# Kernel tuning notes

Hardware: AMD Instinct MI355X
Metric: run time of the kernel (lower is better)

## Reference

```python
import jax, jax.numpy as jnp
import numpy as np

B, D, H, K = 8192, 768, 16384, 32


def _topk_activation(z, k):
    # keep values >= k-th largest per row, zero the rest (dim=1 top-k)
    top_vals = jax.lax.top_k(z, k)[0]          # [B, k]
    thresh = top_vals[:, -1:]                  # [B, 1]
    return jnp.where(z >= thresh, z, jnp.zeros_like(z))


def setup_inputs() -> dict:
    key = jax.random.key(0)
    k1, k2, k3, k4 = jax.random.split(key, 4)
    x = jax.random.normal(k1, (B, D), dtype=jnp.float32)
    # encoder/decoder weights row-normalized as in _init_weights (orthogonal init then F.normalize dim=1)
    W_enc = jax.random.normal(k2, (H, D), dtype=jnp.float32)
    W_enc = W_enc / jnp.linalg.norm(W_enc, axis=1, keepdims=True)
    W_dec = jax.random.normal(k3, (D, H), dtype=jnp.float32)
    W_dec = W_dec / jnp.linalg.norm(W_dec, axis=1, keepdims=True)
    b_pre = 0.01 * jax.random.normal(k4, (D,), dtype=jnp.float32)  # geometric median stand-in
    return {"x": x, "W_enc": W_enc, "W_dec": W_dec, "b_pre": b_pre, "k_sparse": K}


def reference(x, W_enc, W_dec, b_pre, k_sparse):
    # x: [B, D]; single SAE (num_saes=1)
    xc = x - b_pre                                   # subtract pre-bias
    z = jnp.einsum('bd,hd->bh', xc, W_enc)           # encoder (no bias): [B, H]
    encoded = _topk_activation(z, k_sparse)          # top-k sparse hidden
    decoded = jnp.einsum('bh,dh->bd', encoded, W_dec) + b_pre  # decoder + b_pre
    # original returns (hidden_states, reconstructions) lists; num_saes=1
    return (encoded, decoded)
```

## Files before the change

### kernel.cpp

```cpp
#include <hip/hip_runtime.h>
#include <hip/hip_bf16.h>
#include <stdint.h>

#define B_ROWS 8192
#define D_DIM  768
#define H_DIM  16384

typedef _Float16 f16x8 __attribute__((ext_vector_type(8)));
typedef float    f32x4 __attribute__((ext_vector_type(4)));

typedef const __attribute__((address_space(1))) void gas_void;
typedef __attribute__((address_space(3))) void las_void;

union F16U { _Float16 h; unsigned short u; };
union V16U { f16x8 v; uint4 u4; };


#define CAPR   512
#define CUTSIG 2.0f
#define DELTA  1.2e-2f
#define WCAP   48
#define OUTC   64

__global__ __launch_bounds__(256)
void rownorm_kernel(const float* __restrict__ x, const float* __restrict__ bp,
                    float* __restrict__ cut, int* __restrict__ cnt)
{
    const int row = blockIdx.x;
    const int tid = threadIdx.x;
    float v = 0.0f;
    for (int d = tid; d < D_DIM; d += 256) {
        float t = x[(size_t)row * D_DIM + d] - bp[d];
        v += t * t;
    }
#pragma unroll
    for (int off = 32; off >= 1; off >>= 1)
        v += __shfl_down(v, off);
    __shared__ float sw[4];
    if ((tid & 63) == 0) sw[tid >> 6] = v;
    __syncthreads();
    if (tid == 0) {
        cut[row] = CUTSIG * sqrtf((sw[0] + sw[1] + sw[2] + sw[3]) * (1.0f / D_DIM));
        cnt[row] = 0;
    }
}

__global__ __launch_bounds__(256)
void conv_x_kernel(const float* __restrict__ x, const float* __restrict__ bp,
                   _Float16* __restrict__ xo)
{
    size_t e = ((size_t)blockIdx.x * 256 + threadIdx.x) * 8;
    int k = (int)(e % D_DIM);
    float4 a0 = *(const float4*)&x[e];
    float4 a1 = *(const float4*)&x[e + 4];
    float4 b0 = *(const float4*)&bp[k];
    float4 b1 = *(const float4*)&bp[k + 4];
    V16U r;
    r.v[0] = (_Float16)(a0.x - b0.x); r.v[1] = (_Float16)(a0.y - b0.y);
    r.v[2] = (_Float16)(a0.z - b0.z); r.v[3] = (_Float16)(a0.w - b0.w);
    r.v[4] = (_Float16)(a1.x - b1.x); r.v[5] = (_Float16)(a1.y - b1.y);
    r.v[6] = (_Float16)(a1.z - b1.z); r.v[7] = (_Float16)(a1.w - b1.w);
    *(uint4*)&xo[e] = r.u4;
}

__global__ __launch_bounds__(256)
void conv_w_kernel(const float* __restrict__ w, _Float16* __restrict__ wo)
{
    size_t e = ((size_t)blockIdx.x * 256 + threadIdx.x) * 8;
    float4 a0 = *(const float4*)&w[e];
    float4 a1 = *(const float4*)&w[e + 4];
    V16U r;
    r.v[0] = (_Float16)a0.x; r.v[1] = (_Float16)a0.y;
    r.v[2] = (_Float16)a0.z; r.v[3] = (_Float16)a0.w;
    r.v[4] = (_Float16)a1.x; r.v[5] = (_Float16)a1.y;
    r.v[6] = (_Float16)a1.z; r.v[7] = (_Float16)a1.w;
    *(uint4*)&wo[e] = r.u4;
}

__global__ __launch_bounds__(512, 2)
void mfma_gemm_extract(const _Float16* __restrict__ A,
                       const _Float16* __restrict__ Bw,
                       const float* __restrict__ cut,
                       float* __restrict__ z,
                       int* __restrict__ cnt,
                       uint32_t* __restrict__ cand)
{
    __shared__ char smem[65536];

    const int bid = blockIdx.x;
    const int swz = (bid & 7) * 256 + (bid >> 3);
    const int mt  = swz & 31;
    const int nt  = swz >> 5;

    const int tid  = threadIdx.x;
    const int w    = tid >> 6;
    const int lane = tid & 63;
    const int wr   = w >> 2;
    const int wc   = w & 3;

    f32x4 acc[8][4];
#pragma unroll
    for (int i = 0; i < 8; ++i)
#pragma unroll
        for (int j = 0; j < 4; ++j) acc[i][j] = (f32x4)(0.0f);

    const int s_rowin = lane >> 2;
    const size_t s_koff = (size_t)(((lane & 3) ^ ((lane >> 3) & 3))) * 8;

    auto stage = [&](int buf, int k0) {
#pragma unroll
        for (int i = 0; i < 2; ++i) {
            const int grp = w * 2 + i;
            const _Float16* ga = A  + (size_t)(mt * 256 + grp * 16 + s_rowin) * D_DIM + k0 + s_koff;
            const _Float16* gb = Bw + (size_t)(nt * 256 + grp * 16 + s_rowin) * D_DIM + k0 + s_koff;
            __builtin_amdgcn_global_load_lds((gas_void*)ga,
                (las_void*)(smem + buf * 32768 + grp * 1024), 16, 0, 0);
            __builtin_amdgcn_global_load_lds((gas_void*)gb,
                (las_void*)(smem + buf * 32768 + 16384 + grp * 1024), 16, 0, 0);
        }
    };

    const int rslot = (((lane >> 4) ^ ((lane >> 1) & 3)) << 4);
    const int rlow  = lane & 15;

    stage(0, 0);
    __syncthreads();

    int cur = 0;
    for (int t = 0; t < 24; ++t) {
        if (t + 1 < 24) stage(cur ^ 1, (t + 1) * 32);

        const char* bA = smem + cur * 32768;
        const char* bB = bA + 16384;
        f16x8 a[8], b[4];
#pragma unroll
        for (int fi = 0; fi < 8; ++fi)
            a[fi] = *(const f16x8*)(bA + ((wr * 128 + fi * 16 + rlow) << 6) + rslot);
#pragma unroll
        for (int fj = 0; fj < 4; ++fj)
            b[fj] = *(const f16x8*)(bB + ((wc * 64 + fj * 16 + rlow) << 6) + rslot);
#pragma unroll
        for (int fi = 0; fi < 8; ++fi)
#pragma unroll
            for (int fj = 0; fj < 4; ++fj)
                acc[fi][fj] = __builtin_amdgcn_mfma_f32_16x16x32_f16(a[fi], b[fj], acc[fi][fj], 0, 0, 0);

        __syncthreads();
        cur ^= 1;
    }

#pragma unroll
    for (int fi = 0; fi < 8; ++fi) {
        const int grow0 = mt * 256 + wr * 128 + fi * 16 + (lane >> 4) * 4;
        float cut4[4];
#pragma unroll
        for (int q = 0; q < 4; ++q) cut4[q] = cut[grow0 + q];
#pragma unroll
        for (int fj = 0; fj < 4; ++fj) {
            const int gcol = nt * 256 + wc * 64 + fj * 16 + (lane & 15);
#pragma unroll
            for (int q = 0; q < 4; ++q) {
                float val = acc[fi][fj][q];
                if (val >= cut4[q]) {
                    const int grow = grow0 + q;
                    int pos = atomicAdd(&cnt[grow], 1);
                    if (pos < CAPR) {
                        F16U fu; fu.h = (_Float16)val;
                        cand[(size_t)grow * CAPR + pos] =
                            ((uint32_t)fu.u << 16) | (uint32_t)gcol;
                    }
                }
            }
        }
    }

    const float4 z4 = make_float4(0.f, 0.f, 0.f, 0.f);
#pragma unroll
    for (int it = 0; it < 32; ++it) {
        *(float4*)&z[(size_t)(mt * 256 + w + it * 8) * H_DIM + nt * 256 + lane * 4] = z4;
    }
}

__global__ __launch_bounds__(256)
void select_kernel(const float* __restrict__ x,
                   const float* __restrict__ We,
                   const float* __restrict__ bp,
                   const int* __restrict__ cnt,
                   const uint32_t* __restrict__ cand,
                   float* __restrict__ z,
                   int* __restrict__ sel_idx,
                   float* __restrict__ sel_val,
                   int* __restrict__ sel_cnt,
                   const int* __restrict__ kptr)
{
    const int row = blockIdx.x;
    const int tid = threadIdx.x;
    const int K   = min(max(*kptr, 1), OUTC);

    __shared__ float          v[CAPR];
    __shared__ unsigned short hh[CAPR];
    __shared__ unsigned char  csel[CAPR];
    __shared__ float  xs[D_DIM];
    __shared__ int    worig[WCAP];
    __shared__ double wzd[WCAP];
    __shared__ float  sv32;
    __shared__ int    sA, swcnt, snsel;

    if (tid == 0) { sA = 0; swcnt = 0; snsel = 0; }
    const int n = min(cnt[row], CAPR);

    for (int d = tid; d < D_DIM; d += 256) xs[d] = x[(size_t)row * D_DIM + d];

    for (int c = tid; c < n; c += 256) {
        uint32_t p = cand[(size_t)row * CAPR + c];
        F16U fu; fu.u = (unsigned short)(p >> 16);
        v[c]  = (float)fu.h;
        hh[c] = (unsigned short)(p & 0xFFFF);
    }
    __syncthreads();

    if (n <= K) {
        for (int c = tid; c < n; c += 256) csel[c] = 1;
        __syncthreads();
    } else {
        for (int c = tid; c < n; c += 256) {
            float vc = v[c];
            int g = 0, e = 0;
            for (int j = 0; j < n; ++j) {
                float u = v[j];
                g += (u > vc);
                e += (u == vc);
            }
            if (g <= K - 1 && K - 1 < g + e) sv32 = vc;
        }
        __syncthreads();
        const float hi = sv32 + DELTA, lo = sv32 - DELTA;

        for (int c = tid; c < n; c += 256) {
            float vc = v[c];
            unsigned char s = 0;
            if (vc > hi) { s = 1; atomicAdd(&sA, 1); }
            else if (vc >= lo) {
                int m = atomicAdd(&swcnt, 1);
                if (m < WCAP) worig[m] = c;
            }
            csel[c] = s;
        }
        __syncthreads();

        const int wcnt = min(swcnt, WCAP);
        const int wave = tid >> 6;
        const int lane = tid & 63;
        for (int m = wave; m < wcnt; m += 4) {
            const int h = hh[worig[m]];
            const float* wr = We + (size_t)h * D_DIM;
            double s = 0.0;
#pragma unroll
            for (int q = 0; q < 12; ++q) {
                int d = lane * 12 + q;
                s += ((double)xs[d] - (double)bp[d]) * (double)wr[d];
            }
#pragma unroll
            for (int off = 32; off >= 1; off >>= 1)
                s += __shfl_down(s, off);
            if (lane == 0) wzd[m] = s;
        }
        __syncthreads();

        if (tid == 0) {
            int need = K - sA;
            if (need < 0) need = 0;
            if (need > wcnt) need = wcnt;
            for (int m = 0; m < wcnt; ++m) {
                int g = 0;
                for (int j = 0; j < wcnt; ++j) g += (wzd[j] > wzd[m]);
                if (g < need) {
                    csel[worig[m]] = 1;
                    v[worig[m]] = (float)wzd[m];
                }
            }
        }
        __syncthreads();
    }

    for (int c = tid; c < n; c += 256) {
        if (csel[c]) {
            int p = atomicAdd(&snsel, 1);
            if (p < OUTC) {
                const int h = hh[c];
                sel_idx[(size_t)row * OUTC + p] = h;
                sel_val[(size_t)row * OUTC + p] = v[c];
                z[(size_t)row * H_DIM + h] = v[c];
            }
        }
    }
    __syncthreads();
    if (tid == 0) sel_cnt[row] = min(snsel, OUTC);
}

__global__ __launch_bounds__(256)
void transpose_f16_kernel(const float* __restrict__ Wd, _Float16* __restrict__ Wt)
{
    __shared__ float t[32][33];
    const int hb = blockIdx.x * 32;
    const int db = blockIdx.y * 32;
    const int tx = threadIdx.x & 31;
    const int ty = threadIdx.x >> 5;
#pragma unroll
    for (int q = 0; q < 4; ++q)
        t[ty + q * 8][tx] = Wd[(size_t)(db + ty + q * 8) * H_DIM + hb + tx];
    __syncthreads();
#pragma unroll
    for (int q = 0; q < 4; ++q)
        Wt[(size_t)(hb + ty + q * 8) * D_DIM + db + tx] = (_Float16)t[tx][ty + q * 8];
}

__global__ __launch_bounds__(256)
void dec16_kernel(const _Float16* __restrict__ Wt,
                  const int* __restrict__ sel_cnt,
                  const int* __restrict__ sel_idx,
                  const float* __restrict__ sel_val,
                  const float* __restrict__ bp,
                  float* __restrict__ out_dec)
{
    const int row = blockIdx.x;
    const int tid = threadIdx.x;
    __shared__ int   sidx[OUTC];
    __shared__ float sval[OUTC];
    const int c = sel_cnt[row];
    if (tid < c) { sidx[tid] = sel_idx[(size_t)row * OUTC + tid];
                   sval[tid] = sel_val[(size_t)row * OUTC + tid]; }
    __syncthreads();

    float a0 = bp[tid], a1 = bp[tid + 256], a2 = bp[tid + 512];
    for (int k = 0; k < c; ++k) {
        const float vv = sval[k];
        const _Float16* wr = Wt + (size_t)sidx[k] * D_DIM;
        a0 += vv * (float)wr[tid];
        a1 += vv * (float)wr[tid + 256];
        a2 += vv * (float)wr[tid + 512];
    }
    float* o = out_dec + (size_t)row * D_DIM;
    o[tid] = a0; o[tid + 256] = a1; o[tid + 512] = a2;
}


#define BM 128
#define BN 128
#define BK 32

__global__ __launch_bounds__(256)
void enc_gemm_kernel(const float* __restrict__ x,
                     const float* __restrict__ We,
                     const float* __restrict__ bp,
                     float* __restrict__ z)
{
    __shared__ float As[BK][BM + 4];
    __shared__ float Bs[BK][BN + 4];

    const int mt  = blockIdx.x % (B_ROWS / BM);
    const int nt  = blockIdx.x / (B_ROWS / BM);
    const int tid = threadIdx.x;
    const int tx  = tid & 15;
    const int ty  = tid >> 4;
    const int lr = tid >> 3;
    const int lc = (tid & 7) * 4;

    float acc[8][8];
#pragma unroll
    for (int i = 0; i < 8; ++i)
#pragma unroll
        for (int j = 0; j < 8; ++j) acc[i][j] = 0.0f;

    for (int k0 = 0; k0 < D_DIM; k0 += BK) {
        const float4 bp4 = *(const float4*)&bp[k0 + lc];
#pragma unroll
        for (int s = 0; s < 4; ++s) {
            const int r = lr + s * 32;
            float4 a4 = *(const float4*)&x[(size_t)(mt * BM + r) * D_DIM + k0 + lc];
            As[lc + 0][r] = a4.x - bp4.x;
            As[lc + 1][r] = a4.y - bp4.y;
            As[lc + 2][r] = a4.z - bp4.z;
            As[lc + 3][r] = a4.w - bp4.w;
            float4 b4 = *(const float4*)&We[(size_t)(nt * BN + r) * D_DIM + k0 + lc];
            Bs[lc + 0][r] = b4.x;
            Bs[lc + 1][r] = b4.y;
            Bs[lc + 2][r] = b4.z;
            Bs[lc + 3][r] = b4.w;
        }
        __syncthreads();

#pragma unroll 8
        for (int kk = 0; kk < BK; ++kk) {
            float a[8], b[8];
            *(float4*)&a[0] = *(const float4*)&As[kk][ty * 4];
            *(float4*)&a[4] = *(const float4*)&As[kk][64 + ty * 4];
            *(float4*)&b[0] = *(const float4*)&Bs[kk][tx * 4];
            *(float4*)&b[4] = *(const float4*)&Bs[kk][64 + tx * 4];
#pragma unroll
            for (int i = 0; i < 8; ++i)
#pragma unroll
                for (int j = 0; j < 8; ++j)
                    acc[i][j] += a[i] * b[j];
        }
        __syncthreads();
    }

#pragma unroll
    for (int i = 0; i < 8; ++i) {
        const int rloc = (i < 4) ? (ty * 4 + i) : (64 + ty * 4 + (i - 4));
        const size_t row = (size_t)(mt * BM + rloc);
        float4 v0 = make_float4(acc[i][0], acc[i][1], acc[i][2], acc[i][3]);
        float4 v1 = make_float4(acc[i][4], acc[i][5], acc[i][6], acc[i][7]);
        *(float4*)&z[row * H_DIM + nt * BN + tx * 4]      = v0;
        *(float4*)&z[row * H_DIM + nt * BN + 64 + tx * 4] = v1;
    }
}

#define CAP  1024
#define WCAP3 64

__global__ __launch_bounds__(256)
void topk_kernel(float* __restrict__ z,
                 const float* __restrict__ x,
                 const float* __restrict__ We,
                 const float* __restrict__ bp,
                 int* __restrict__ ws_cnt,
                 int* __restrict__ ws_idx,
                 float* __restrict__ ws_val,
                 const int* __restrict__ kptr)
{
    const int row = blockIdx.x;
    const int tid = threadIdx.x;
    const int K   = min(max(*kptr, 1), OUTC);
    float* zr = z + (size_t)row * H_DIM;

    __shared__ float cval[CAP];
    __shared__ int   cidx[CAP];
    __shared__ unsigned char csel3[CAP];
    __shared__ int   worig3[WCAP3];
    __shared__ double wzd3[WCAP3];
    __shared__ int   oidx[OUTC];
    __shared__ float oval[OUTC];
    __shared__ int   scount, swcnt3, sA3, souts;
    __shared__ float sv32f;

    if (tid == 0) { scount = 0; swcnt3 = 0; sA3 = 0; souts = 0; }
    __syncthreads();

    for (int j4 = tid; j4 < H_DIM / 4; j4 += 256) {
        float4 v4 = ((const float4*)zr)[j4];
        float vs[4] = {v4.x, v4.y, v4.z, v4.w};
#pragma unroll
        for (int c = 0; c < 4; ++c) {
            if (vs[c] >= 2.0f) {
                int p = atomicAdd(&scount, 1);
                if (p < CAP) { cval[p] = vs[c]; cidx[p] = j4 * 4 + c; }
            }
        }
    }
    __syncthreads();
    const int n3 = min(scount, CAP);

    if (n3 <= K) {
        for (int c = tid; c < n3; c += 256) csel3[c] = 1;
        __syncthreads();
    } else {
        for (int c = tid; c < n3; c += 256) {
            float vv = cval[c];
            int g = 0, e = 0;
            for (int j = 0; j < n3; ++j) {
                float u = cval[j];
                g += (u > vv);
                e += (u == vv);
            }
            if (g <= K - 1 && K - 1 < g + e) sv32f = vv;
        }
        __syncthreads();

        const float D3 = 1e-4f;
        const float hi = sv32f + D3, lo = sv32f - D3;
        for (int c = tid; c < n3; c += 256) {
            float vv = cval[c];
            unsigned char s = 0;
            if (vv > hi) { s = 1; atomicAdd(&sA3, 1); }
            else if (vv >= lo) {
                int m = atomicAdd(&swcnt3, 1);
                if (m < WCAP3) worig3[m] = c;
            }
            csel3[c] = s;
        }
        __syncthreads();

        const int wcnt = min(swcnt3, WCAP3);
        const int wave = tid >> 6;
        const int lane = tid & 63;
        for (int m = wave; m < wcnt; m += 4) {
            const int h = cidx[worig3[m]];
            const float* wr = We + (size_t)h * D_DIM;
            const float* xr = x + (size_t)row * D_DIM;
            double s = 0.0;
#pragma unroll
            for (int q = 0; q < 12; ++q) {
                int d = lane * 12 + q;
                s += ((double)xr[d] - (double)bp[d]) * (double)wr[d];
            }
#pragma unroll
            for (int off = 32; off >= 1; off >>= 1)
                s += __shfl_down(s, off);
            if (lane == 0) wzd3[m] = s;
        }
        __syncthreads();

        if (tid == 0) {
            int need = K - sA3;
            if (need < 0) need = 0;
            if (need > wcnt) need = wcnt;
            for (int m = 0; m < wcnt; ++m) {
                int g = 0;
                for (int j = 0; j < wcnt; ++j) g += (wzd3[j] > wzd3[m]);
                if (g < need) csel3[worig3[m]] = 1;
            }
        }
        __syncthreads();
    }

    for (int c = tid; c < n3; c += 256) {
        if (csel3[c]) {
            int p = atomicAdd(&souts, 1);
            if (p < OUTC) { oidx[p] = cidx[c]; oval[p] = cval[c]; }
        }
    }
    __syncthreads();
    const int outs = min(souts, OUTC);

    for (int j4 = tid; j4 < H_DIM / 4; j4 += 256)
        ((float4*)zr)[j4] = make_float4(0.f, 0.f, 0.f, 0.f);
    __syncthreads();
    if (tid < outs) {
        zr[oidx[tid]] = oval[tid];
        ws_idx[row * OUTC + tid] = oidx[tid];
        ws_val[row * OUTC + tid] = oval[tid];
    }
    if (tid == 0) ws_cnt[row] = outs;
}

__global__ __launch_bounds__(256)
void transpose_kernel(const float* __restrict__ Wd, float* __restrict__ Wt)
{
    __shared__ float t[32][33];
    const int hb = blockIdx.x * 32;
    const int db = blockIdx.y * 32;
    const int tx = threadIdx.x & 31;
    const int ty = threadIdx.x >> 5;
#pragma unroll
    for (int q = 0; q < 4; ++q)
        t[ty + q * 8][tx] = Wd[(size_t)(db + ty + q * 8) * H_DIM + hb + tx];
    __syncthreads();
#pragma unroll
    for (int q = 0; q < 4; ++q)
        Wt[(size_t)(hb + ty + q * 8) * D_DIM + db + tx] = t[tx][ty + q * 8];
}

template <bool WT>
__global__ __launch_bounds__(256)
void dec_kernel(const float* __restrict__ W,
                const int* __restrict__ ws_cnt,
                const int* __restrict__ ws_idx,
                const float* __restrict__ ws_val,
                const float* __restrict__ bp,
                float* __restrict__ out_dec)
{
    const int row = blockIdx.x;
    const int tid = threadIdx.x;
    __shared__ int   sidx[OUTC];
    __shared__ float sval[OUTC];
    const int cnt = ws_cnt[row];
    if (tid < cnt) { sidx[tid] = ws_idx[row * OUTC + tid]; sval[tid] = ws_val[row * OUTC + tid]; }
    __syncthreads();

    float a0 = bp[tid], a1 = bp[tid + 256], a2 = bp[tid + 512];
    for (int k = 0; k < cnt; ++k) {
        const float vv = sval[k];
        const int h = sidx[k];
        if (WT) {
            const float* wr = W + (size_t)h * D_DIM;
            a0 += vv * wr[tid];
            a1 += vv * wr[tid + 256];
            a2 += vv * wr[tid + 512];
        } else {
            a0 += vv * W[(size_t)(tid)       * H_DIM + h];
            a1 += vv * W[(size_t)(tid + 256) * H_DIM + h];
            a2 += vv * W[(size_t)(tid + 512) * H_DIM + h];
        }
    }
    float* o = out_dec + (size_t)row * D_DIM;
    o[tid] = a0; o[tid + 256] = a1; o[tid + 512] = a2;
}

extern "C" void kernel_launch(void* const* d_in, const int* in_sizes, int n_in,
                              void* d_out, int out_size, void* d_ws, size_t ws_size,
                              hipStream_t stream)
{
    const float* x    = (const float*)d_in[0];
    const float* We   = (const float*)d_in[1];
    const float* Wd   = (const float*)d_in[2];
    const float* bp   = (const float*)d_in[3];
    const int*   kptr = (const int*)d_in[4];

    float* out_enc = (float*)d_out;
    float* out_dec = out_enc + (size_t)B_ROWS * H_DIM;
    char*  ws      = (char*)d_ws;

    const size_t xc16_b = (size_t)B_ROWS * D_DIM * 2;
    const size_t we16_b = (size_t)H_DIM * D_DIM * 2;
    const size_t conv_b = xc16_b + we16_b;
    const size_t cand_b = (size_t)B_ROWS * CAPR * 4;
    const size_t cnt_b  = (size_t)B_ROWS * 4;
    const size_t cut_b  = (size_t)B_ROWS * 4;
    const size_t sidx_b = (size_t)B_ROWS * OUTC * 4;
    const size_t sval_b = (size_t)B_ROWS * OUTC * 4;
    const size_t scnt_b = (size_t)B_ROWS * 4;
    const size_t new_req = conv_b + cand_b + cnt_b + cut_b + sidx_b + sval_b + scnt_b;

    if (ws_size >= new_req) {
        _Float16* xc16 = (_Float16*)ws;
        _Float16* we16 = (_Float16*)(ws + xc16_b);
        _Float16* wt16 = (_Float16*)ws;
        size_t off = conv_b;
        uint32_t* cand = (uint32_t*)(ws + off); off += cand_b;
        int*   cnt     = (int*)(ws + off);      off += cnt_b;
        float* cutv    = (float*)(ws + off);    off += cut_b;
        int*   sidx    = (int*)(ws + off);      off += sidx_b;
        float* sval    = (float*)(ws + off);    off += sval_b;
        int*   scnt    = (int*)(ws + off);

        hipLaunchKernelGGL(rownorm_kernel, dim3(B_ROWS), dim3(256), 0, stream, x, bp, cutv, cnt);
        hipLaunchKernelGGL(conv_x_kernel, dim3(B_ROWS * D_DIM / 2048), dim3(256), 0, stream,
                           x, bp, xc16);
        hipLaunchKernelGGL(conv_w_kernel, dim3(H_DIM * D_DIM / 2048), dim3(256), 0, stream,
                           We, we16);
        hipLaunchKernelGGL(mfma_gemm_extract, dim3(2048), dim3(512), 0, stream,
                           xc16, we16, cutv, out_enc, cnt, cand);
        hipLaunchKernelGGL(transpose_f16_kernel, dim3(H_DIM / 32, D_DIM / 32), dim3(256),
                           0, stream, Wd, wt16);
        hipLaunchKernelGGL(select_kernel, dim3(B_ROWS), dim3(256), 0, stream,
                           x, We, bp, cnt, cand, out_enc, sidx, sval, scnt, kptr);
        hipLaunchKernelGGL(dec16_kernel, dim3(B_ROWS), dim3(256), 0, stream,
                           wt16, scnt, sidx, sval, bp, out_dec);
        return;
    }

    const size_t wt_bytes  = (size_t)H_DIM * D_DIM * sizeof(float);
    const size_t idx_bytes = (size_t)B_ROWS * OUTC * sizeof(int);
    const size_t val_bytes = (size_t)B_ROWS * OUTC * sizeof(float);
    const size_t cnt_bytes = (size_t)B_ROWS * sizeof(int);
    const bool use_wt = (ws_size >= wt_bytes + idx_bytes + val_bytes + cnt_bytes);

    float* Wt; int* ws_idx; float* ws_val; int* ws_cnt;
    size_t off = 0;
    if (use_wt) { Wt = (float*)(ws + off); off += wt_bytes; } else { Wt = nullptr; }
    ws_idx = (int*)(ws + off);   off += idx_bytes;
    ws_val = (float*)(ws + off); off += val_bytes;
    ws_cnt = (int*)(ws + off);   off += cnt_bytes;

    if (use_wt) {
        hipLaunchKernelGGL(transpose_kernel, dim3(H_DIM / 32, D_DIM / 32), dim3(256),
                           0, stream, Wd, Wt);
    }
    hipLaunchKernelGGL(enc_gemm_kernel,
                       dim3((B_ROWS / BM) * (H_DIM / BN)), dim3(256), 0, stream,
                       x, We, bp, out_enc);
    hipLaunchKernelGGL(topk_kernel, dim3(B_ROWS), dim3(256), 0, stream,
                       out_enc, x, We, bp, ws_cnt, ws_idx, ws_val, kptr);
    if (use_wt) {
        hipLaunchKernelGGL((dec_kernel<true>), dim3(B_ROWS), dim3(256), 0, stream,
                           Wt, ws_cnt, ws_idx, ws_val, bp, out_dec);
    } else {
        hipLaunchKernelGGL((dec_kernel<false>), dim3(B_ROWS), dim3(256), 0, stream,
                           Wd, ws_cnt, ws_idx, ws_val, bp, out_dec);
    }
}
```

Measured before the change: 819.2 us.

## Fuse x conversion with row norm and restructure GEMM staging pipeline

Merges the row-norm kernel and the fp16 conversion of x into one kernel, so x is read once and one launch is dropped. The GEMM main loop now keeps two tiles in flight: it issues two stages up front, waits on vmcnt with explicit barriers, issues the next load right after the LDS reads, and raises wave priority around the MFMA block. This aims to hide global-to-LDS latency behind compute. It relies on hand-written waitcnt counts matching the four loads per stage, which is fragile if the compiler reorders or changes the load count.

```diff
diff --git a/kernel.cpp b/kernel.cpp
--- a/kernel.cpp
+++ b/kernel.cpp
@@ -17,21 +17,26 @@
 
 
 #define CAPR   512
-#define CUTSIG 2.0f
 #define DELTA  1.2e-2f
 #define WCAP   48
 #define OUTC   64
 
 __global__ __launch_bounds__(256)
-void rownorm_kernel(const float* __restrict__ x, const float* __restrict__ bp,
-                    float* __restrict__ cut, int* __restrict__ cnt)
+void conv_x_norm_kernel(const float* __restrict__ x, const float* __restrict__ bp,
+                        _Float16* __restrict__ xo, float* __restrict__ cut,
+                        int* __restrict__ cnt)
 {
     const int row = blockIdx.x;
     const int tid = threadIdx.x;
+    const float* xr = x + (size_t)row * D_DIM;
+    _Float16* xow = xo + (size_t)row * D_DIM;
     float v = 0.0f;
-    for (int d = tid; d < D_DIM; d += 256) {
-        float t = x[(size_t)row * D_DIM + d] - bp[d];
+#pragma unroll
+    for (int q = 0; q < 3; ++q) {
+        const int d = tid + q * 256;
+        float t = xr[d] - bp[d];
         v += t * t;
+        xow[d] = (_Float16)t;
     }
 #pragma unroll
     for (int off = 32; off >= 1; off >>= 1)
@@ -40,27 +45,9 @@
     if ((tid & 63) == 0) sw[tid >> 6] = v;
     __syncthreads();
     if (tid == 0) {
-        cut[row] = CUTSIG * sqrtf((sw[0] + sw[1] + sw[2] + sw[3]) * (1.0f / D_DIM));
+        cut[row] = 2.0f * sqrtf((sw[0] + sw[1] + sw[2] + sw[3]) * (1.0f / D_DIM));
         cnt[row] = 0;
     }
-}
-
-__global__ __launch_bounds__(256)
-void conv_x_kernel(const float* __restrict__ x, const float* __restrict__ bp,
-                   _Float16* __restrict__ xo)
-{
-    size_t e = ((size_t)blockIdx.x * 256 + threadIdx.x) * 8;
-    int k = (int)(e % D_DIM);
-    float4 a0 = *(const float4*)&x[e];
-    float4 a1 = *(const float4*)&x[e + 4];
-    float4 b0 = *(const float4*)&bp[k];
-    float4 b1 = *(const float4*)&bp[k + 4];
-    V16U r;
-    r.v[0] = (_Float16)(a0.x - b0.x); r.v[1] = (_Float16)(a0.y - b0.y);
-    r.v[2] = (_Float16)(a0.z - b0.z); r.v[3] = (_Float16)(a0.w - b0.w);
-    r.v[4] = (_Float16)(a1.x - b1.x); r.v[5] = (_Float16)(a1.y - b1.y);
-    r.v[6] = (_Float16)(a1.z - b1.z); r.v[7] = (_Float16)(a1.w - b1.w);
-    *(uint4*)&xo[e] = r.u4;
 }
 
 __global__ __launch_bounds__(256)
@@ -107,7 +94,9 @@
     const int s_rowin = lane >> 2;
     const size_t s_koff = (size_t)(((lane & 3) ^ ((lane >> 3) & 3))) * 8;
 
-    auto stage = [&](int buf, int k0) {
+    auto stage = [&](int tile) {
+        const int buf = tile & 1;
+        const int k0  = tile * 32;
 #pragma unroll
         for (int i = 0; i < 2; ++i) {
             const int grp = w * 2 + i;
@@ -123,14 +112,15 @@
     const int rslot = (((lane >> 4) ^ ((lane >> 1) & 3)) << 4);
     const int rlow  = lane & 15;
 
-    stage(0, 0);
-    __syncthreads();
-
-    int cur = 0;
+    stage(0);
+    stage(1);
+
     for (int t = 0; t < 24; ++t) {
-        if (t + 1 < 24) stage(cur ^ 1, (t + 1) * 32);
-
-        const char* bA = smem + cur * 32768;
+        if (t < 23) asm volatile("s_waitcnt vmcnt(4)" ::: "memory");
+        else        asm volatile("s_waitcnt vmcnt(0)" ::: "memory");
+        __builtin_amdgcn_s_barrier();
+
+        const char* bA = smem + (t & 1) * 32768;
         const char* bB = bA + 16384;
         f16x8 a[8], b[4];
 #pragma unroll
@@ -139,14 +129,20 @@
 #pragma unroll
         for (int fj = 0; fj < 4; ++fj)
             b[fj] = *(const f16x8*)(bB + ((wc * 64 + fj * 16 + rlow) << 6) + rslot);
+
+        asm volatile("s_waitcnt lgkmcnt(0)" ::: "memory");
+        __builtin_amdgcn_sched_barrier(0);
+        __builtin_amdgcn_s_barrier();
+
+        if (t + 2 < 24) stage(t + 2);
+
+        __builtin_amdgcn_s_setprio(1);
 #pragma unroll
         for (int fi = 0; fi < 8; ++fi)
 #pragma unroll
             for (int fj = 0; fj < 4; ++fj)
                 acc[fi][fj] = __builtin_amdgcn_mfma_f32_16x16x32_f16(a[fi], b[fj], acc[fi][fj], 0, 0, 0);
-
-        __syncthreads();
-        cur ^= 1;
+        __builtin_amdgcn_s_setprio(0);
     }
 
 #pragma unroll
@@ -635,9 +631,8 @@
         float* sval    = (float*)(ws + off);    off += sval_b;
         int*   scnt    = (int*)(ws + off);
 
-        hipLaunchKernelGGL(rownorm_kernel, dim3(B_ROWS), dim3(256), 0, stream, x, bp, cutv, cnt);
-        hipLaunchKernelGGL(conv_x_kernel, dim3(B_ROWS * D_DIM / 2048), dim3(256), 0, stream,
-                           x, bp, xc16);
+        hipLaunchKernelGGL(conv_x_norm_kernel, dim3(B_ROWS), dim3(256), 0, stream,
+                           x, bp, xc16, cutv, cnt);
         hipLaunchKernelGGL(conv_w_kernel, dim3(H_DIM * D_DIM / 2048), dim3(256), 0, stream,
                            We, we16);
         hipLaunchKernelGGL(mfma_gemm_extract, dim3(2048), dim3(512), 0, stream,
```

After: 820.4 us. Within noise of the previous version (+0.1%).
